# Performance work log

Measured on AMD Instinct MI355X. Metric: run time of the kernel, lower is better.

The kernel has to match this reference:

```python
import jax, jax.numpy as jnp
import numpy as np

SEQ_LENS = [1024, 768, 512, 896, 640, 384, 1024, 896]
TOTAL = sum(SEQ_LENS)  # 6144
EMBED = 768
NUM_HEADS = 12
HEAD_DIM = EMBED // NUM_HEADS
FFN = 3072
LN_EPS = 1e-5


def _pad_maps():
    # static (numpy) index maps for ragged <-> padded layout
    B, S = len(SEQ_LENS), max(SEQ_LENS)
    offs = np.cumsum([0] + SEQ_LENS)
    pad_idx = np.zeros((B, S), np.int32)
    valid = np.zeros((B, S), bool)
    for i, L in enumerate(SEQ_LENS):
        pad_idx[i, :L] = np.arange(offs[i], offs[i] + L)
        valid[i, :L] = True
    flat_b = np.concatenate([np.full(L, i, np.int32) for i, L in enumerate(SEQ_LENS)])
    flat_p = np.concatenate([np.arange(L, dtype=np.int32) for L in SEQ_LENS])
    return jnp.asarray(pad_idx), jnp.asarray(valid), jnp.asarray(flat_b), jnp.asarray(flat_p)

PAD_IDX, VALID, FLAT_B, FLAT_P = _pad_maps()


def _layernorm(x, g, b):
    mu = jnp.mean(x, axis=-1, keepdims=True)
    var = jnp.mean(jnp.square(x - mu), axis=-1, keepdims=True)
    return (x - mu) * jax.lax.rsqrt(var + LN_EPS) * g + b


def setup_inputs() -> dict:
    key = jax.random.key(0)
    ks = jax.random.split(key, 8)
    return {
        "hidden_states": jax.random.normal(ks[0], (TOTAL, EMBED), jnp.float32),
        "attention_mask": jnp.ones((TOTAL,), jnp.int32),
        "in_proj_w": 0.02 * jax.random.normal(ks[1], (3 * EMBED, EMBED), jnp.float32),
        "in_proj_b": jnp.zeros((3 * EMBED,), jnp.float32),
        "out_proj_w": 0.02 * jax.random.normal(ks[2], (EMBED, EMBED), jnp.float32),
        "out_proj_b": jnp.zeros((EMBED,), jnp.float32),
        "ln1_g": jnp.ones((EMBED,), jnp.float32),
        "ln1_b": jnp.zeros((EMBED,), jnp.float32),
        "fc1_w": 0.02 * jax.random.normal(ks[3], (FFN, EMBED), jnp.float32),
        "fc1_b": jnp.zeros((FFN,), jnp.float32),
        "fc2_w": 0.02 * jax.random.normal(ks[4], (EMBED, FFN), jnp.float32),
        "fc2_b": jnp.zeros((EMBED,), jnp.float32),
        "ln2_g": jnp.ones((EMBED,), jnp.float32),
        "ln2_b": jnp.zeros((EMBED,), jnp.float32),
    }


def reference(hidden_states, attention_mask, in_proj_w, in_proj_b, out_proj_w,
              out_proj_b, ln1_g, ln1_b, fc1_w, fc1_b, fc2_w, fc2_b, ln2_g, ln2_b):
    B, S = PAD_IDX.shape
    residual = hidden_states
    x = _layernorm(hidden_states, ln1_g, ln1_b)  # pre-LN (do_layer_norm_before)

    # ragged -> padded [B, S, E]; key validity combines padding mask and ragged tail
    xp = x[PAD_IDX]
    key_valid = VALID & (attention_mask[PAD_IDX] != 0)

    # fused QKV projection (nn.MultiheadAttention in_proj)
    qkv = xp @ in_proj_w.T + in_proj_b  # [B, S, 3E]
    q, k, v = jnp.split(qkv, 3, axis=-1)
    q = q.reshape(B, S, NUM_HEADS, HEAD_DIM) * (1.0 / np.sqrt(HEAD_DIM))
    k = k.reshape(B, S, NUM_HEADS, HEAD_DIM)
    v = v.reshape(B, S, NUM_HEADS, HEAD_DIM)

    scores = jnp.einsum('bqhd,bkhd->bhqk', q, k)  # [B, H, S, S]
    causal = jnp.tril(jnp.ones((S, S), bool))
    mask = causal[None, None] & key_valid[:, None, None, :]
    scores = jnp.where(mask, scores, jnp.float32(-1e30))
    probs = jax.nn.softmax(scores, axis=-1)
    ctx = jnp.einsum('bhqk,bkhd->bqhd', probs, v).reshape(B, S, EMBED)
    attn = ctx @ out_proj_w.T + out_proj_b

    # padded -> ragged, residual
    h = residual + attn[FLAT_B, FLAT_P]

    # FFN block (pre-LN)
    residual = h
    h = _layernorm(h, ln2_g, ln2_b)
    h = jax.nn.relu(h @ fc1_w.T + fc1_b)
    h = h @ fc2_w.T + fc2_b
    return residual + h
```

## Files before the change

kernel.cpp:

```cpp
#include <hip/hip_runtime.h>
#include <hip/hip_bf16.h>

#define TOTAL 6144
#define EMBED 768
#define QKV3  2304
#define FFN   3072
#define NH    12
#define HD    64

typedef unsigned short u16;
typedef unsigned int u32;
typedef float f32x4 __attribute__((ext_vector_type(4)));
typedef __bf16 bf16x8 __attribute__((ext_vector_type(8)));

__device__ __constant__ int BOFF[9] = {0, 1024, 1792, 2304, 3200, 3840, 4224, 5248, 6144};

__device__ __forceinline__ float b2f(u16 h) {
    union { u32 u; float f; } v; v.u = ((u32)h) << 16; return v.f;
}
__device__ __forceinline__ u16 f2b(float f) {
    union { u32 u; float f; } v; v.f = f;
    u32 u = v.u + 0x7fffu + ((v.u >> 16) & 1u);
    return (u16)(u >> 16);
}

__device__ __forceinline__ void gload_lds16(const u16* g, u16* l) {
    __builtin_amdgcn_global_load_lds(
        (const __attribute__((address_space(1))) u32*)(uintptr_t)g,
        (__attribute__((address_space(3))) u32*)(uintptr_t)l, 16, 0, 0);
}

__device__ __forceinline__ float rowmax16(float x) {
    int v;
    v = __builtin_amdgcn_mov_dpp(__float_as_int(x), 0xB1, 0xF, 0xF, true);
    x = fmaxf(x, __int_as_float(v));
    v = __builtin_amdgcn_mov_dpp(__float_as_int(x), 0x4E, 0xF, 0xF, true);
    x = fmaxf(x, __int_as_float(v));
    v = __builtin_amdgcn_mov_dpp(__float_as_int(x), 0x124, 0xF, 0xF, true);
    x = fmaxf(x, __int_as_float(v));
    v = __builtin_amdgcn_mov_dpp(__float_as_int(x), 0x128, 0xF, 0xF, true);
    x = fmaxf(x, __int_as_float(v));
    return x;
}

__global__ void cvt4_kernel(const float* __restrict__ s0, u16* __restrict__ d0, int n0,
                            const float* __restrict__ s1, u16* __restrict__ d1, int n1,
                            const float* __restrict__ s2, u16* __restrict__ d2, int n2,
                            const float* __restrict__ s3, u16* __restrict__ d3, int n3) {
    int i = blockIdx.x * blockDim.x + threadIdx.x;
    const float* s;
    u16* d;
    int j = i;
    if (j < n0) { s = s0; d = d0; }
    else {
        j -= n0;
        if (j < n1) { s = s1; d = d1; }
        else {
            j -= n1;
            if (j < n2) { s = s2; d = d2; }
            else {
                j -= n2;
                if (j >= n3) return;
                s = s3; d = d3;
            }
        }
    }
    float4 v = ((const float4*)s)[j];
    ushort4 o;
    o.x = f2b(v.x); o.y = f2b(v.y); o.z = f2b(v.z); o.w = f2b(v.w);
    ((ushort4*)d)[j] = o;
}

__global__ __launch_bounds__(256) void ln_kernel(const float* __restrict__ x,
                                                 const float* __restrict__ g,
                                                 const float* __restrict__ b,
                                                 u16* __restrict__ out) {
    int row = blockIdx.x * 4 + (threadIdx.x >> 6);
    int lane = threadIdx.x & 63;
    const float* xr = x + (size_t)row * EMBED;
    float4 v[3];
    float s = 0.f, sq = 0.f;
#pragma unroll
    for (int c = 0; c < 3; ++c) {
        v[c] = *(const float4*)(xr + c * 256 + lane * 4);
        s += v[c].x + v[c].y + v[c].z + v[c].w;
        sq += v[c].x * v[c].x + v[c].y * v[c].y + v[c].z * v[c].z + v[c].w * v[c].w;
    }
#pragma unroll
    for (int o = 32; o; o >>= 1) {
        s += __shfl_xor(s, o);
        sq += __shfl_xor(sq, o);
    }
    float mu = s * (1.f / 768.f);
    float var = sq * (1.f / 768.f) - mu * mu;
    float rs = rsqrtf(var + 1e-5f);
    u16* orow = out + (size_t)row * EMBED;
#pragma unroll
    for (int c = 0; c < 3; ++c) {
        int col = c * 256 + lane * 4;
        float4 gg = *(const float4*)(g + col);
        float4 bb = *(const float4*)(b + col);
        ushort4 o;
        o.x = f2b((v[c].x - mu) * rs * gg.x + bb.x);
        o.y = f2b((v[c].y - mu) * rs * gg.y + bb.y);
        o.z = f2b((v[c].z - mu) * rs * gg.z + bb.z);
        o.w = f2b((v[c].w - mu) * rs * gg.w + bb.w);
        *(ushort4*)(orow + col) = o;
    }
}

template <int RELU, int RES, int OUTB, int OUTF>
__global__ __launch_bounds__(256) void gemm128(const u16* __restrict__ A,
                                               const u16* __restrict__ B,
                                               const float* __restrict__ bias,
                                               const float* __restrict__ res,
                                               u16* __restrict__ outb,
                                               float* __restrict__ outf,
                                               int M, int N, int K) {
    __shared__ u16 As[2][128][64];
    __shared__ u16 Bs[2][128][64];
    int t = threadIdx.x;
    int lane = t & 63, w = t >> 6;
    int wr = w >> 1, wc = w & 1;
    int gx = gridDim.x;
    int nwg = gx * gridDim.y;
    int flat = blockIdx.y * gx + blockIdx.x;
    int swz = (flat & 7) * (nwg >> 3) + (flat >> 3);
    int m0 = (swz / gx) * 128, n0 = (swz % gx) * 128;
    int lr = lane >> 3;
    int lcg = (lane & 7) ^ (lr & 7);
    int c16 = lane & 15, hi = lane >> 4;

    f32x4 acc[4][4];
#pragma unroll
    for (int m = 0; m < 4; ++m)
#pragma unroll
        for (int n = 0; n < 4; ++n) acc[m][n] = (f32x4)0.f;

    const u16* Ab = A + (size_t)(m0 + w * 32 + lr) * K + lcg * 8;
    const u16* Bb = B + (size_t)(n0 + w * 32 + lr) * K + lcg * 8;

    int nk = K >> 6;
#pragma unroll
    for (int i = 0; i < 4; ++i) {
        gload_lds16(Ab + (size_t)(i * 8) * K, &As[0][w * 32 + i * 8][0]);
        gload_lds16(Bb + (size_t)(i * 8) * K, &Bs[0][w * 32 + i * 8][0]);
    }

    for (int tk = 0; tk < nk; ++tk) {
        int cur = tk & 1;
        if (tk + 1 < nk) {
            int k1 = (tk + 1) << 6;
#pragma unroll
            for (int i = 0; i < 4; ++i) {
                gload_lds16(Ab + (size_t)(i * 8) * K + k1, &As[cur ^ 1][w * 32 + i * 8][0]);
                gload_lds16(Bb + (size_t)(i * 8) * K + k1, &Bs[cur ^ 1][w * 32 + i * 8][0]);
            }
            asm volatile("s_waitcnt vmcnt(8)" ::: "memory");
        } else {
            asm volatile("s_waitcnt vmcnt(0)" ::: "memory");
        }
        __builtin_amdgcn_sched_barrier(0);
        __builtin_amdgcn_s_barrier();
#pragma unroll
        for (int ks = 0; ks < 2; ++ks) {
            bf16x8 af[4], bfr[4];
#pragma unroll
            for (int m = 0; m < 4; ++m)
                af[m] = *(const bf16x8*)&As[cur][wr * 64 + m * 16 + c16][((ks * 4 + hi) ^ (c16 & 7)) * 8];
#pragma unroll
            for (int n = 0; n < 4; ++n)
                bfr[n] = *(const bf16x8*)&Bs[cur][wc * 64 + n * 16 + c16][((ks * 4 + hi) ^ (c16 & 7)) * 8];
#pragma unroll
            for (int m = 0; m < 4; ++m)
#pragma unroll
                for (int n = 0; n < 4; ++n)
                    acc[m][n] = __builtin_amdgcn_mfma_f32_16x16x32_bf16(af[m], bfr[n], acc[m][n], 0, 0, 0);
        }
        asm volatile("s_waitcnt lgkmcnt(0)" ::: "memory");
        __builtin_amdgcn_sched_barrier(0);
        __builtin_amdgcn_s_barrier();
    }

#pragma unroll
    for (int m = 0; m < 4; ++m)
#pragma unroll
        for (int n = 0; n < 4; ++n) {
            int cg = n0 + wc * 64 + n * 16 + c16;
            float bv = bias[cg];
#pragma unroll
            for (int j = 0; j < 4; ++j) {
                int rg = m0 + wr * 64 + m * 16 + hi * 4 + j;
                float v = acc[m][n][j] + bv;
                if (RELU) v = fmaxf(v, 0.f);
                if (RES) v += res[(size_t)rg * N + cg];
                if (OUTB) outb[(size_t)rg * N + cg] = f2b(v);
                if (OUTF) outf[(size_t)rg * N + cg] = v;
            }
        }
}

__global__ __launch_bounds__(256) void vtrans_kernel(const u16* __restrict__ qkv,
                                                     u16* __restrict__ vT) {
    __shared__ u16 T[64][64];
    int t = threadIdx.x;
    int r0 = blockIdx.x * 64;
    int d0 = blockIdx.y * 64;
#pragma unroll
    for (int s = 0; s < 2; ++s) {
        int idx = s * 256 + t;
        int r = idx >> 3, cg = idx & 7;
        uint4 v = *(const uint4*)&qkv[(size_t)(r0 + r) * QKV3 + 2 * EMBED + d0 + cg * 8];
        int sw = (((r & 7) ^ ((r >> 3) & 7)) << 3);
        *(uint4*)&T[r][(cg * 8) ^ sw] = v;
    }
    __syncthreads();
#pragma unroll
    for (int s = 0; s < 2; ++s) {
        int idx = s * 256 + t;
        int gd = idx >> 3, rc = idx & 7;
        u16 tmp[8];
#pragma unroll
        for (int j = 0; j < 8; ++j) {
            int row = rc * 8 + j;
            int sw = (((row & 7) ^ ((row >> 3) & 7)) << 3);
            tmp[j] = T[row][gd ^ sw];
        }
        *(uint4*)&vT[(size_t)(d0 + gd) * TOTAL + r0 + rc * 8] = *(uint4*)tmp;
    }
}

__global__ __launch_bounds__(64, 2) void attn_mfma(const u16* __restrict__ qkv,
                                                   const u16* __restrict__ vT,
                                                   const int* __restrict__ amask,
                                                   u16* __restrict__ ctx) {
    __shared__ u16 Pl[32][64];
    int l = threadIdx.x;
    int Q = l >> 4, c = l & 15;
    int bid = blockIdx.x;
    int swz = (bid & 7) * 288 + (bid >> 3);
    int h = swz / 192;
    int qt = 191 - (swz % 192);
    int r0 = qt * 32;
    int b = 0;
#pragma unroll
    for (int i = 0; i < 8; ++i)
        if (r0 >= BOFF[i + 1]) b = i + 1;
    int boff = BOFF[b];
    int p0 = r0 - boff;
    int nk = p0 + 32;
    const float SCALE = 0.125f * 1.44269504f;

    bf16x8 qa[2][2];
#pragma unroll
    for (int m = 0; m < 2; ++m)
#pragma unroll
        for (int ks = 0; ks < 2; ++ks)
            qa[m][ks] = *(const bf16x8*)&qkv[(size_t)(r0 + m * 16 + c) * QKV3 + h * HD + ks * 32 + Q * 8];

    bf16x8 vones;
#pragma unroll
    for (int j = 0; j < 8; ++j) vones[j] = (__bf16)1.0f;

    f32x4 oacc[2][4], lacc[2];
    float mrun[2][4];
#pragma unroll
    for (int m = 0; m < 2; ++m) {
        lacc[m] = (f32x4)0.f;
#pragma unroll
        for (int nt = 0; nt < 4; ++nt) oacc[m][nt] = (f32x4)0.f;
#pragma unroll
        for (int r = 0; r < 4; ++r) mrun[m][r] = -1e30f;
    }

    for (int k0 = 0; k0 < nk; k0 += 64) {
        bf16x8 kb[2][4], vb[2][4];
#pragma unroll
        for (int ks = 0; ks < 2; ++ks)
#pragma unroll
            for (int nt = 0; nt < 4; ++nt) {
                kb[ks][nt] = *(const bf16x8*)&qkv[(size_t)(boff + k0 + nt * 16 + c) * QKV3 +
                                                  EMBED + h * HD + ks * 32 + Q * 8];
                vb[ks][nt] = *(const bf16x8*)&vT[(size_t)(h * HD + nt * 16 + c) * TOTAL +
                                                 boff + k0 + ks * 32 + Q * 8];
            }

        f32x4 sacc[2][4];
#pragma unroll
        for (int m = 0; m < 2; ++m)
#pragma unroll
            for (int nt = 0; nt < 4; ++nt) sacc[m][nt] = (f32x4)0.f;
#pragma unroll
        for (int ks = 0; ks < 2; ++ks)
#pragma unroll
            for (int m = 0; m < 2; ++m)
#pragma unroll
                for (int nt = 0; nt < 4; ++nt)
                    sacc[m][nt] = __builtin_amdgcn_mfma_f32_16x16x32_bf16(qa[m][ks], kb[ks][nt], sacc[m][nt], 0, 0, 0);

        int am[4];
#pragma unroll
        for (int nt = 0; nt < 4; ++nt) am[nt] = amask[boff + k0 + nt * 16 + c];
#pragma unroll
        for (int m = 0; m < 2; ++m)
#pragma unroll
            for (int nt = 0; nt < 4; ++nt) {
                int kpos = k0 + nt * 16 + c;
                float madd = am[nt] ? 0.f : -1e30f;
#pragma unroll
                for (int r = 0; r < 4; ++r) {
                    float s = fmaf(sacc[m][nt][r], SCALE, madd);
                    int qp = p0 + m * 16 + 4 * Q + r;
                    sacc[m][nt][r] = (kpos <= qp) ? s : -1e30f;
                }
            }

        float mx[2][4];
        int small = 1;
#pragma unroll
        for (int m = 0; m < 2; ++m)
#pragma unroll
            for (int r = 0; r < 4; ++r) {
                float v = fmaxf(fmaxf(sacc[m][0][r], sacc[m][1][r]),
                                fmaxf(sacc[m][2][r], sacc[m][3][r]));
                v = rowmax16(v);
                mx[m][r] = v;
                small &= (v <= mrun[m][r]) ? 1 : 0;
            }
        if (!__all(small)) {
#pragma unroll
            for (int m = 0; m < 2; ++m)
#pragma unroll
                for (int r = 0; r < 4; ++r) {
                    float mn = fmaxf(mrun[m][r], mx[m][r]);
                    float f = exp2f(mrun[m][r] - mn);
                    mrun[m][r] = mn;
                    lacc[m][r] *= f;
#pragma unroll
                    for (int nt = 0; nt < 4; ++nt) oacc[m][nt][r] *= f;
                }
        }

#pragma unroll
        for (int m = 0; m < 2; ++m)
#pragma unroll
            for (int nt = 0; nt < 4; ++nt)
#pragma unroll
                for (int r = 0; r < 4; ++r) {
                    float p = exp2f(sacc[m][nt][r] - mrun[m][r]);
                    int row = m * 16 + 4 * Q + r;
                    int cch = ((nt * 2 + (c >> 3)) ^ (row & 7)) << 3;
                    Pl[row][cch + (c & 7)] = f2b(p);
                }

#pragma unroll
        for (int ks = 0; ks < 2; ++ks) {
            bf16x8 pa[2];
#pragma unroll
            for (int m = 0; m < 2; ++m)
                pa[m] = *(const bf16x8*)&Pl[m * 16 + c][(((ks * 4 + Q) ^ (c & 7)) << 3)];
#pragma unroll
            for (int m = 0; m < 2; ++m) {
                lacc[m] = __builtin_amdgcn_mfma_f32_16x16x32_bf16(pa[m], vones, lacc[m], 0, 0, 0);
#pragma unroll
                for (int nt = 0; nt < 4; ++nt)
                    oacc[m][nt] = __builtin_amdgcn_mfma_f32_16x16x32_bf16(pa[m], vb[ks][nt], oacc[m][nt], 0, 0, 0);
            }
        }
    }

#pragma unroll
    for (int m = 0; m < 2; ++m)
#pragma unroll
        for (int r = 0; r < 4; ++r) {
            float inv = 1.0f / lacc[m][r];
#pragma unroll
            for (int nt = 0; nt < 4; ++nt)
                ctx[(size_t)(r0 + m * 16 + 4 * Q + r) * EMBED + h * HD + nt * 16 + c] =
                    f2b(oacc[m][nt][r] * inv);
        }
}

extern "C" void kernel_launch(void* const* d_in, const int* in_sizes, int n_in,
                              void* d_out, int out_size, void* d_ws, size_t ws_size,
                              hipStream_t stream) {
    (void)in_sizes; (void)n_in; (void)out_size; (void)ws_size;
    const float* hidden = (const float*)d_in[0];
    const int*   amask  = (const int*)d_in[1];
    const float* in_w   = (const float*)d_in[2];
    const float* in_b   = (const float*)d_in[3];
    const float* out_w  = (const float*)d_in[4];
    const float* out_b  = (const float*)d_in[5];
    const float* ln1g   = (const float*)d_in[6];
    const float* ln1b   = (const float*)d_in[7];
    const float* fc1w   = (const float*)d_in[8];
    const float* fc1b   = (const float*)d_in[9];
    const float* fc2w   = (const float*)d_in[10];
    const float* fc2b   = (const float*)d_in[11];
    const float* ln2g   = (const float*)d_in[12];
    const float* ln2b   = (const float*)d_in[13];
    float* out = (float*)d_out;

    char* ws = (char*)d_ws;
    size_t off = 0;
    auto alloc = [&](size_t bytes) {
        void* p = ws + off;
        off += (bytes + 255) & ~(size_t)255;
        return p;
    };
    u16* w_in_bf  = (u16*)alloc((size_t)QKV3 * EMBED * 2);
    u16* w_out_bf = (u16*)alloc((size_t)EMBED * EMBED * 2);
    u16* w_fc1_bf = (u16*)alloc((size_t)FFN * EMBED * 2);
    u16* w_fc2_bf = (u16*)alloc((size_t)EMBED * FFN * 2);
    u16* xln  = (u16*)alloc((size_t)TOTAL * EMBED * 2);
    u16* qkv  = (u16*)alloc((size_t)TOTAL * QKV3 * 2);
    u16* ctx  = (u16*)alloc((size_t)TOTAL * EMBED * 2);
    float* hmid = (float*)alloc((size_t)TOTAL * EMBED * 4);
    u16* hln  = (u16*)alloc((size_t)TOTAL * EMBED * 2);
    u16* f1o  = (u16*)alloc((size_t)TOTAL * FFN * 2);
    u16* vT   = xln;

    cvt4_kernel<<<6912, 256, 0, stream>>>(in_w, w_in_bf, 442368,
                                          out_w, w_out_bf, 147456,
                                          fc1w, w_fc1_bf, 589824,
                                          fc2w, w_fc2_bf, 589824);

    ln_kernel<<<TOTAL / 4, 256, 0, stream>>>(hidden, ln1g, ln1b, xln);
    gemm128<0, 0, 1, 0><<<dim3(QKV3 / 128, TOTAL / 128), 256, 0, stream>>>(
        xln, w_in_bf, in_b, nullptr, qkv, nullptr, TOTAL, QKV3, EMBED);
    vtrans_kernel<<<dim3(TOTAL / 64, EMBED / 64), 256, 0, stream>>>(qkv, vT);
    attn_mfma<<<dim3((TOTAL / 32) * NH), 64, 0, stream>>>(qkv, vT, amask, ctx);
    gemm128<0, 1, 0, 1><<<dim3(EMBED / 128, TOTAL / 128), 256, 0, stream>>>(
        ctx, w_out_bf, out_b, hidden, nullptr, hmid, TOTAL, EMBED, EMBED);
    ln_kernel<<<TOTAL / 4, 256, 0, stream>>>(hmid, ln2g, ln2b, hln);
    gemm128<1, 0, 1, 0><<<dim3(FFN / 128, TOTAL / 128), 256, 0, stream>>>(
        hln, w_fc1_bf, fc1b, nullptr, f1o, nullptr, TOTAL, FFN, EMBED);
    gemm128<0, 1, 0, 1><<<dim3(EMBED / 128, TOTAL / 128), 256, 0, stream>>>(
        f1o, w_fc2_bf, fc2b, hmid, nullptr, out, TOTAL, EMBED, FFN);
}
```

Measured before the change: 227.3 us.

## Split attention key loop across four waves with LDS softmax combine

Attention blocks grow from one wave to four. Each wave processes an interleaved subset of 64-key chunks with its own online-softmax state. Partial outputs, running maxima and sums are then merged through shared memory before writing the context. The goal is to shorten the serial key loop for long causal rows and expose more parallelism per query tile. In exchange it adds a reduction step, two barriers and about 35KB of LDS per block, and leaves waves idle on short tiles.

```diff
diff --git a/kernel.cpp b/kernel.cpp
--- a/kernel.cpp
+++ b/kernel.cpp
@@ -230,12 +230,21 @@
     }
 }
 
-__global__ __launch_bounds__(64, 2) void attn_mfma(const u16* __restrict__ qkv,
-                                                   const u16* __restrict__ vT,
-                                                   const int* __restrict__ amask,
-                                                   u16* __restrict__ ctx) {
-    __shared__ u16 Pl[32][64];
-    int l = threadIdx.x;
+struct CombineBufs {
+    float om[4][64][33];
+    float ml[4][32][2];
+};
+union AttnLds {
+    u16 pl[4][32][64];
+    CombineBufs c;
+};
+
+__global__ __launch_bounds__(256) void attn_mfma(const u16* __restrict__ qkv,
+                                                 const u16* __restrict__ vT,
+                                                 const int* __restrict__ amask,
+                                                 u16* __restrict__ ctx) {
+    __shared__ AttnLds S;
+    int t = threadIdx.x, l = t & 63, w = t >> 6;
     int Q = l >> 4, c = l & 15;
     int bid = blockIdx.x;
     int swz = (bid & 7) * 288 + (bid >> 3);
@@ -273,7 +282,8 @@
         for (int r = 0; r < 4; ++r) mrun[m][r] = -1e30f;
     }
 
-    for (int k0 = 0; k0 < nk; k0 += 64) {
+    for (int kc = w; (kc << 6) < nk; kc += 4) {
+        int k0 = kc << 6;
         bf16x8 kb[2][4], vb[2][4];
 #pragma unroll
         for (int ks = 0; ks < 2; ++ks)
@@ -350,7 +360,7 @@
                     float p = exp2f(sacc[m][nt][r] - mrun[m][r]);
                     int row = m * 16 + 4 * Q + r;
                     int cch = ((nt * 2 + (c >> 3)) ^ (row & 7)) << 3;
-                    Pl[row][cch + (c & 7)] = f2b(p);
+                    S.pl[w][row][cch + (c & 7)] = f2b(p);
                 }
 
 #pragma unroll
@@ -358,7 +368,7 @@
             bf16x8 pa[2];
 #pragma unroll
             for (int m = 0; m < 2; ++m)
-                pa[m] = *(const bf16x8*)&Pl[m * 16 + c][(((ks * 4 + Q) ^ (c & 7)) << 3)];
+                pa[m] = *(const bf16x8*)&S.pl[w][m * 16 + c][(((ks * 4 + Q) ^ (c & 7)) << 3)];
 #pragma unroll
             for (int m = 0; m < 2; ++m) {
                 lacc[m] = __builtin_amdgcn_mfma_f32_16x16x32_bf16(pa[m], vones, lacc[m], 0, 0, 0);
@@ -369,16 +379,52 @@
         }
     }
 
+    __syncthreads();
 #pragma unroll
     for (int m = 0; m < 2; ++m)
 #pragma unroll
+        for (int nt = 0; nt < 4; ++nt)
+            *(f32x4*)&S.c.om[w][nt * 16 + c][m * 16 + 4 * Q] = oacc[m][nt];
+    if (c == 0) {
+#pragma unroll
+        for (int m = 0; m < 2; ++m)
+#pragma unroll
+            for (int r = 0; r < 4; ++r) {
+                int row = m * 16 + 4 * Q + r;
+                S.c.ml[w][row][0] = mrun[m][r];
+                S.c.ml[w][row][1] = lacc[m][r];
+            }
+    }
+    __syncthreads();
+
+#pragma unroll
+    for (int m = 0; m < 2; ++m) {
+        int rbase = m * 16 + 4 * Q;
+        float Mm[4], ll[4];
+#pragma unroll
         for (int r = 0; r < 4; ++r) {
-            float inv = 1.0f / lacc[m][r];
-#pragma unroll
-            for (int nt = 0; nt < 4; ++nt)
-                ctx[(size_t)(r0 + m * 16 + 4 * Q + r) * EMBED + h * HD + nt * 16 + c] =
-                    f2b(oacc[m][nt][r] * inv);
-        }
+            float mm = -1e30f;
+#pragma unroll
+            for (int wv = 0; wv < 4; ++wv) mm = fmaxf(mm, S.c.ml[wv][rbase + r][0]);
+            Mm[r] = mm;
+            float lt = 0.f;
+#pragma unroll
+            for (int wv = 0; wv < 4; ++wv)
+                lt += exp2f(S.c.ml[wv][rbase + r][0] - mm) * S.c.ml[wv][rbase + r][1];
+            ll[r] = lt;
+        }
+        f32x4 o = (f32x4)0.f;
+#pragma unroll
+        for (int wv = 0; wv < 4; ++wv) {
+            f32x4 ov = *(const f32x4*)&S.c.om[wv][w * 16 + c][rbase];
+#pragma unroll
+            for (int r = 0; r < 4; ++r)
+                o[r] += exp2f(S.c.ml[wv][rbase + r][0] - Mm[r]) * ov[r];
+        }
+#pragma unroll
+        for (int r = 0; r < 4; ++r)
+            ctx[(size_t)(r0 + rbase + r) * EMBED + h * HD + w * 16 + c] = f2b(o[r] / ll[r]);
+    }
 }
 
 extern "C" void kernel_launch(void* const* d_in, const int* in_sizes, int n_in,
@@ -429,7 +475,7 @@
     gemm128<0, 0, 1, 0><<<dim3(QKV3 / 128, TOTAL / 128), 256, 0, stream>>>(
         xln, w_in_bf, in_b, nullptr, qkv, nullptr, TOTAL, QKV3, EMBED);
     vtrans_kernel<<<dim3(TOTAL / 64, EMBED / 64), 256, 0, stream>>>(qkv, vT);
-    attn_mfma<<<dim3((TOTAL / 32) * NH), 64, 0, stream>>>(qkv, vT, amask, ctx);
+    attn_mfma<<<dim3((TOTAL / 32) * NH), 256, 0, stream>>>(qkv, vT, amask, ctx);
     gemm128<0, 1, 0, 1><<<dim3(EMBED / 128, TOTAL / 128), 256, 0, stream>>>(
         ctx, w_out_bf, out_b, hidden, nullptr, hmid, TOTAL, EMBED, EMBED);
     ln_kernel<<<TOTAL / 4, 256, 0, stream>>>(hmid, ln2g, ln2b, hln);
```

Result: no change. 230.3 us (+1.3%).

## Double-buffer K/V loads in attention, bitpack mask, skip causal masking on full chunks

Applied to the files above, without the earlier changes.

Restructures the attention inner loop to prefetch the next K/V chunk into a second register set while the current chunk computes. The int attention mask is packed into bitmasks by a new small kernel, and mask and causal work is skipped on chunks that lie fully below the diagonal when no keys are masked. The scale is folded into the exp2 argument, and the row sum comes from DPP reductions instead of an extra MFMA with a ones vector. The bf16 conversion now uses the native cast. Prefetching doubles the K/V register footprint, which may raise register pressure and hurt occupancy.

```diff
diff --git a/kernel.cpp b/kernel.cpp
--- a/kernel.cpp
+++ b/kernel.cpp
@@ -15,13 +15,9 @@
 
 __device__ __constant__ int BOFF[9] = {0, 1024, 1792, 2304, 3200, 3840, 4224, 5248, 6144};
 
-__device__ __forceinline__ float b2f(u16 h) {
-    union { u32 u; float f; } v; v.u = ((u32)h) << 16; return v.f;
-}
 __device__ __forceinline__ u16 f2b(float f) {
-    union { u32 u; float f; } v; v.f = f;
-    u32 u = v.u + 0x7fffu + ((v.u >> 16) & 1u);
-    return (u16)(u >> 16);
+    __bf16 h = (__bf16)f;
+    return __builtin_bit_cast(u16, h);
 }
 
 __device__ __forceinline__ void gload_lds16(const u16* g, u16* l) {
@@ -40,6 +36,18 @@
     x = fmaxf(x, __int_as_float(v));
     v = __builtin_amdgcn_mov_dpp(__float_as_int(x), 0x128, 0xF, 0xF, true);
     x = fmaxf(x, __int_as_float(v));
+    return x;
+}
+__device__ __forceinline__ float rowsum16(float x) {
+    int v;
+    v = __builtin_amdgcn_mov_dpp(__float_as_int(x), 0xB1, 0xF, 0xF, true);
+    x += __int_as_float(v);
+    v = __builtin_amdgcn_mov_dpp(__float_as_int(x), 0x4E, 0xF, 0xF, true);
+    x += __int_as_float(v);
+    v = __builtin_amdgcn_mov_dpp(__float_as_int(x), 0x124, 0xF, 0xF, true);
+    x += __int_as_float(v);
+    v = __builtin_amdgcn_mov_dpp(__float_as_int(x), 0x128, 0xF, 0xF, true);
+    x += __int_as_float(v);
     return x;
 }
 
@@ -69,6 +77,15 @@
     ushort4 o;
     o.x = f2b(v.x); o.y = f2b(v.y); o.z = f2b(v.z); o.w = f2b(v.w);
     ((ushort4*)d)[j] = o;
+}
+
+__global__ void maskbits_kernel(const int* __restrict__ am, u32* __restrict__ mb) {
+    int i = blockIdx.x * 64 + threadIdx.x;
+    unsigned long long bal = __ballot(am[i] != 0);
+    if (threadIdx.x == 0) {
+        mb[blockIdx.x * 2] = (u32)bal;
+        mb[blockIdx.x * 2 + 1] = (u32)(bal >> 32);
+    }
 }
 
 __global__ __launch_bounds__(256) void ln_kernel(const float* __restrict__ x,
@@ -232,11 +249,11 @@
 
 __global__ __launch_bounds__(64, 2) void attn_mfma(const u16* __restrict__ qkv,
                                                    const u16* __restrict__ vT,
-                                                   const int* __restrict__ amask,
+                                                   const u32* __restrict__ mbits,
                                                    u16* __restrict__ ctx) {
     __shared__ u16 Pl[32][64];
     int l = threadIdx.x;
-    int Q = l >> 4, c = l & 15;
+    int hi = l >> 4, c = l & 15;
     int bid = blockIdx.x;
     int swz = (bid & 7) * 288 + (bid >> 3);
     int h = swz / 192;
@@ -248,7 +265,8 @@
         if (r0 >= BOFF[i + 1]) b = i + 1;
     int boff = BOFF[b];
     int p0 = r0 - boff;
-    int nk = p0 + 32;
+    int nchunks = (p0 >> 6) + 1;
+    int nfull = (p0 >= 63) ? (((p0 - 63) >> 6) + 1) : 0;
     const float SCALE = 0.125f * 1.44269504f;
 
     bf16x8 qa[2][2];
@@ -256,35 +274,40 @@
     for (int m = 0; m < 2; ++m)
 #pragma unroll
         for (int ks = 0; ks < 2; ++ks)
-            qa[m][ks] = *(const bf16x8*)&qkv[(size_t)(r0 + m * 16 + c) * QKV3 + h * HD + ks * 32 + Q * 8];
-
-    bf16x8 vones;
-#pragma unroll
-    for (int j = 0; j < 8; ++j) vones[j] = (__bf16)1.0f;
-
-    f32x4 oacc[2][4], lacc[2];
-    float mrun[2][4];
-#pragma unroll
-    for (int m = 0; m < 2; ++m) {
-        lacc[m] = (f32x4)0.f;
+            qa[m][ks] = *(const bf16x8*)&qkv[(size_t)(r0 + m * 16 + c) * QKV3 + h * HD + ks * 32 + hi * 8];
+
+    f32x4 oacc[2][4];
+    float lacc[2][4], mrun[2][4];
+#pragma unroll
+    for (int m = 0; m < 2; ++m)
+#pragma unroll
+        for (int r = 0; r < 4; ++r) {
+            lacc[m][r] = 0.f;
+            mrun[m][r] = -1e30f;
+        }
+#pragma unroll
+    for (int m = 0; m < 2; ++m)
 #pragma unroll
         for (int nt = 0; nt < 4; ++nt) oacc[m][nt] = (f32x4)0.f;
-#pragma unroll
-        for (int r = 0; r < 4; ++r) mrun[m][r] = -1e30f;
-    }
-
-    for (int k0 = 0; k0 < nk; k0 += 64) {
-        bf16x8 kb[2][4], vb[2][4];
+
+    auto loadc = [&](int kc, bf16x8 (&kb)[2][4], bf16x8 (&vb)[2][4], u32 (&mw)[2]) {
+        int k0 = kc << 6;
 #pragma unroll
         for (int ks = 0; ks < 2; ++ks)
 #pragma unroll
             for (int nt = 0; nt < 4; ++nt) {
                 kb[ks][nt] = *(const bf16x8*)&qkv[(size_t)(boff + k0 + nt * 16 + c) * QKV3 +
-                                                  EMBED + h * HD + ks * 32 + Q * 8];
+                                                  EMBED + h * HD + ks * 32 + hi * 8];
                 vb[ks][nt] = *(const bf16x8*)&vT[(size_t)(h * HD + nt * 16 + c) * TOTAL +
-                                                 boff + k0 + ks * 32 + Q * 8];
+                                                 boff + k0 + ks * 32 + hi * 8];
             }
-
+        int wi = (boff + k0) >> 5;
+        mw[0] = mbits[wi];
+        mw[1] = mbits[wi + 1];
+    };
+
+    auto body = [&](int kc, bf16x8 (&kb)[2][4], bf16x8 (&vb)[2][4], u32 (&mw)[2]) {
+        int k0 = kc << 6;
         f32x4 sacc[2][4];
 #pragma unroll
         for (int m = 0; m < 2; ++m)
@@ -298,22 +321,31 @@
                 for (int nt = 0; nt < 4; ++nt)
                     sacc[m][nt] = __builtin_amdgcn_mfma_f32_16x16x32_bf16(qa[m][ks], kb[ks][nt], sacc[m][nt], 0, 0, 0);
 
-        int am[4];
-#pragma unroll
-        for (int nt = 0; nt < 4; ++nt) am[nt] = amask[boff + k0 + nt * 16 + c];
-#pragma unroll
-        for (int m = 0; m < 2; ++m)
-#pragma unroll
-            for (int nt = 0; nt < 4; ++nt) {
-                int kpos = k0 + nt * 16 + c;
-                float madd = am[nt] ? 0.f : -1e30f;
-#pragma unroll
-                for (int r = 0; r < 4; ++r) {
-                    float s = fmaf(sacc[m][nt][r], SCALE, madd);
-                    int qp = p0 + m * 16 + 4 * Q + r;
-                    sacc[m][nt][r] = (kpos <= qp) ? s : -1e30f;
+        bool fullmask = ((mw[0] & mw[1]) == 0xFFFFFFFFu);
+        if (kc >= nfull) {
+#pragma unroll
+            for (int m = 0; m < 2; ++m)
+#pragma unroll
+                for (int nt = 0; nt < 4; ++nt) {
+                    int kpos = k0 + nt * 16 + c;
+                    float madd = fullmask ? 0.f
+                        : (((mw[nt >> 1] >> (((nt & 1) << 4) + c)) & 1u) ? 0.f : -1e30f);
+#pragma unroll
+                    for (int r = 0; r < 4; ++r) {
+                        int qp = p0 + m * 16 + 4 * hi + r;
+                        sacc[m][nt][r] = (kpos <= qp) ? (sacc[m][nt][r] + madd) : -1e30f;
+                    }
                 }
-            }
+        } else if (!fullmask) {
+#pragma unroll
+            for (int m = 0; m < 2; ++m)
+#pragma unroll
+                for (int nt = 0; nt < 4; ++nt) {
+                    float madd = ((mw[nt >> 1] >> (((nt & 1) << 4) + c)) & 1u) ? 0.f : -1e30f;
+#pragma unroll
+                    for (int r = 0; r < 4; ++r) sacc[m][nt][r] += madd;
+                }
+        }
 
         float mx[2][4];
         int small = 1;
@@ -333,7 +365,7 @@
 #pragma unroll
                 for (int r = 0; r < 4; ++r) {
                     float mn = fmaxf(mrun[m][r], mx[m][r]);
-                    float f = exp2f(mrun[m][r] - mn);
+                    float f = exp2f((mrun[m][r] - mn) * SCALE);
                     mrun[m][r] = mn;
                     lacc[m][r] *= f;
 #pragma unroll
@@ -341,32 +373,58 @@
                 }
         }
 
+        float negm[2][4];
 #pragma unroll
         for (int m = 0; m < 2; ++m)
 #pragma unroll
+            for (int r = 0; r < 4; ++r) negm[m][r] = -mrun[m][r] * SCALE;
+        float psum[2][4];
+#pragma unroll
+        for (int m = 0; m < 2; ++m)
+#pragma unroll
+            for (int r = 0; r < 4; ++r) psum[m][r] = 0.f;
+#pragma unroll
+        for (int m = 0; m < 2; ++m)
+#pragma unroll
             for (int nt = 0; nt < 4; ++nt)
 #pragma unroll
                 for (int r = 0; r < 4; ++r) {
-                    float p = exp2f(sacc[m][nt][r] - mrun[m][r]);
-                    int row = m * 16 + 4 * Q + r;
+                    float p = exp2f(fmaf(sacc[m][nt][r], SCALE, negm[m][r]));
+                    psum[m][r] += p;
+                    int row = m * 16 + 4 * hi + r;
                     int cch = ((nt * 2 + (c >> 3)) ^ (row & 7)) << 3;
                     Pl[row][cch + (c & 7)] = f2b(p);
                 }
+#pragma unroll
+        for (int m = 0; m < 2; ++m)
+#pragma unroll
+            for (int r = 0; r < 4; ++r) lacc[m][r] += rowsum16(psum[m][r]);
 
 #pragma unroll
         for (int ks = 0; ks < 2; ++ks) {
             bf16x8 pa[2];
 #pragma unroll
             for (int m = 0; m < 2; ++m)
-                pa[m] = *(const bf16x8*)&Pl[m * 16 + c][(((ks * 4 + Q) ^ (c & 7)) << 3)];
-#pragma unroll
-            for (int m = 0; m < 2; ++m) {
-                lacc[m] = __builtin_amdgcn_mfma_f32_16x16x32_bf16(pa[m], vones, lacc[m], 0, 0, 0);
+                pa[m] = *(const bf16x8*)&Pl[m * 16 + c][(((ks * 4 + hi) ^ (c & 7)) << 3)];
+#pragma unroll
+            for (int m = 0; m < 2; ++m)
 #pragma unroll
                 for (int nt = 0; nt < 4; ++nt)
                     oacc[m][nt] = __builtin_amdgcn_mfma_f32_16x16x32_bf16(pa[m], vb[ks][nt], oacc[m][nt], 0, 0, 0);
-            }
-        }
+        }
+    };
+
+    bf16x8 kbA[2][4], vbA[2][4], kbB[2][4], vbB[2][4];
+    u32 mwA[2], mwB[2];
+    loadc(0, kbA, vbA, mwA);
+    int kc = 0;
+    while (true) {
+        if (kc + 1 < nchunks) loadc(kc + 1, kbB, vbB, mwB);
+        body(kc, kbA, vbA, mwA);
+        if (++kc >= nchunks) break;
+        if (kc + 1 < nchunks) loadc(kc + 1, kbA, vbA, mwA);
+        body(kc, kbB, vbB, mwB);
+        if (++kc >= nchunks) break;
     }
 
 #pragma unroll
@@ -376,7 +434,7 @@
             float inv = 1.0f / lacc[m][r];
 #pragma unroll
             for (int nt = 0; nt < 4; ++nt)
-                ctx[(size_t)(r0 + m * 16 + 4 * Q + r) * EMBED + h * HD + nt * 16 + c] =
+                ctx[(size_t)(r0 + m * 16 + 4 * hi + r) * EMBED + h * HD + nt * 16 + c] =
                     f2b(oacc[m][nt][r] * inv);
         }
 }
@@ -418,18 +476,20 @@
     float* hmid = (float*)alloc((size_t)TOTAL * EMBED * 4);
     u16* hln  = (u16*)alloc((size_t)TOTAL * EMBED * 2);
     u16* f1o  = (u16*)alloc((size_t)TOTAL * FFN * 2);
+    u32* mbits = (u32*)alloc(192 * 4);
     u16* vT   = xln;
 
     cvt4_kernel<<<6912, 256, 0, stream>>>(in_w, w_in_bf, 442368,
                                           out_w, w_out_bf, 147456,
                                           fc1w, w_fc1_bf, 589824,
                                           fc2w, w_fc2_bf, 589824);
+    maskbits_kernel<<<96, 64, 0, stream>>>(amask, mbits);
 
     ln_kernel<<<TOTAL / 4, 256, 0, stream>>>(hidden, ln1g, ln1b, xln);
     gemm128<0, 0, 1, 0><<<dim3(QKV3 / 128, TOTAL / 128), 256, 0, stream>>>(
         xln, w_in_bf, in_b, nullptr, qkv, nullptr, TOTAL, QKV3, EMBED);
     vtrans_kernel<<<dim3(TOTAL / 64, EMBED / 64), 256, 0, stream>>>(qkv, vT);
-    attn_mfma<<<dim3((TOTAL / 32) * NH), 64, 0, stream>>>(qkv, vT, amask, ctx);
+    attn_mfma<<<dim3((TOTAL / 32) * NH), 64, 0, stream>>>(qkv, vT, mbits, ctx);
     gemm128<0, 1, 0, 1><<<dim3(EMBED / 128, TOTAL / 128), 256, 0, stream>>>(
         ctx, w_out_bf, out_b, hidden, nullptr, hmid, TOTAL, EMBED, EMBED);
     ln_kernel<<<TOTAL / 4, 256, 0, stream>>>(hmid, ln2g, ln2b, hln);
```

New measurement: 266.7 us. +17.3%, slower.

## Fuse V transpose into QKV GEMM epilogue and bitpack attention mask

Applied to the files above, without the earlier changes.

Removes the separate V-transpose kernel by having the QKV GEMM epilogue write V transposed directly into a spare buffer. Precomputes the attention mask as bitwords with a ballot kernel, and skips causal and mask arithmetic for fully-below-diagonal chunks when the mask word is all ones. It also folds the softmax scale into the exp2 FMA and uses the hardware bf16 conversion. The cost is scattered 8-byte strided stores in the GEMM epilogue and an extra tiny launch.

```diff
diff --git a/kernel.cpp b/kernel.cpp
--- a/kernel.cpp
+++ b/kernel.cpp
@@ -15,13 +15,9 @@
 
 __device__ __constant__ int BOFF[9] = {0, 1024, 1792, 2304, 3200, 3840, 4224, 5248, 6144};
 
-__device__ __forceinline__ float b2f(u16 h) {
-    union { u32 u; float f; } v; v.u = ((u32)h) << 16; return v.f;
-}
 __device__ __forceinline__ u16 f2b(float f) {
-    union { u32 u; float f; } v; v.f = f;
-    u32 u = v.u + 0x7fffu + ((v.u >> 16) & 1u);
-    return (u16)(u >> 16);
+    __bf16 h = (__bf16)f;
+    return __builtin_bit_cast(u16, h);
 }
 
 __device__ __forceinline__ void gload_lds16(const u16* g, u16* l) {
@@ -71,6 +67,15 @@
     ((ushort4*)d)[j] = o;
 }
 
+__global__ void maskbits_kernel(const int* __restrict__ am, u32* __restrict__ mb) {
+    int i = blockIdx.x * 64 + threadIdx.x;
+    unsigned long long bal = __ballot(am[i] != 0);
+    if (threadIdx.x == 0) {
+        mb[blockIdx.x * 2] = (u32)bal;
+        mb[blockIdx.x * 2 + 1] = (u32)(bal >> 32);
+    }
+}
+
 __global__ __launch_bounds__(256) void ln_kernel(const float* __restrict__ x,
                                                  const float* __restrict__ g,
                                                  const float* __restrict__ b,
@@ -109,13 +114,14 @@
     }
 }
 
-template <int RELU, int RES, int OUTB, int OUTF>
+template <int RELU, int RES, int OUTB, int OUTF, int VTR>
 __global__ __launch_bounds__(256) void gemm128(const u16* __restrict__ A,
                                                const u16* __restrict__ B,
                                                const float* __restrict__ bias,
                                                const float* __restrict__ res,
                                                u16* __restrict__ outb,
                                                float* __restrict__ outf,
+                                               u16* __restrict__ vout,
                                                int M, int N, int K) {
     __shared__ u16 As[2][128][64];
     __shared__ u16 Bs[2][128][64];
@@ -188,55 +194,33 @@
         for (int n = 0; n < 4; ++n) {
             int cg = n0 + wc * 64 + n * 16 + c16;
             float bv = bias[cg];
+            float vj[4];
 #pragma unroll
             for (int j = 0; j < 4; ++j) {
                 int rg = m0 + wr * 64 + m * 16 + hi * 4 + j;
                 float v = acc[m][n][j] + bv;
                 if (RELU) v = fmaxf(v, 0.f);
                 if (RES) v += res[(size_t)rg * N + cg];
+                vj[j] = v;
                 if (OUTB) outb[(size_t)rg * N + cg] = f2b(v);
                 if (OUTF) outf[(size_t)rg * N + cg] = v;
             }
-        }
-}
-
-__global__ __launch_bounds__(256) void vtrans_kernel(const u16* __restrict__ qkv,
-                                                     u16* __restrict__ vT) {
-    __shared__ u16 T[64][64];
-    int t = threadIdx.x;
-    int r0 = blockIdx.x * 64;
-    int d0 = blockIdx.y * 64;
-#pragma unroll
-    for (int s = 0; s < 2; ++s) {
-        int idx = s * 256 + t;
-        int r = idx >> 3, cg = idx & 7;
-        uint4 v = *(const uint4*)&qkv[(size_t)(r0 + r) * QKV3 + 2 * EMBED + d0 + cg * 8];
-        int sw = (((r & 7) ^ ((r >> 3) & 7)) << 3);
-        *(uint4*)&T[r][(cg * 8) ^ sw] = v;
-    }
-    __syncthreads();
-#pragma unroll
-    for (int s = 0; s < 2; ++s) {
-        int idx = s * 256 + t;
-        int gd = idx >> 3, rc = idx & 7;
-        u16 tmp[8];
-#pragma unroll
-        for (int j = 0; j < 8; ++j) {
-            int row = rc * 8 + j;
-            int sw = (((row & 7) ^ ((row >> 3) & 7)) << 3);
-            tmp[j] = T[row][gd ^ sw];
-        }
-        *(uint4*)&vT[(size_t)(d0 + gd) * TOTAL + r0 + rc * 8] = *(uint4*)tmp;
-    }
+            if (VTR && cg >= 2 * EMBED) {
+                ushort4 tv;
+                tv.x = f2b(vj[0]); tv.y = f2b(vj[1]); tv.z = f2b(vj[2]); tv.w = f2b(vj[3]);
+                int rgb = m0 + wr * 64 + m * 16 + hi * 4;
+                *(ushort4*)&vout[(size_t)(cg - 2 * EMBED) * TOTAL + rgb] = tv;
+            }
+        }
 }
 
 __global__ __launch_bounds__(64, 2) void attn_mfma(const u16* __restrict__ qkv,
                                                    const u16* __restrict__ vT,
-                                                   const int* __restrict__ amask,
+                                                   const u32* __restrict__ mbits,
                                                    u16* __restrict__ ctx) {
     __shared__ u16 Pl[32][64];
     int l = threadIdx.x;
-    int Q = l >> 4, c = l & 15;
+    int hi = l >> 4, c = l & 15;
     int bid = blockIdx.x;
     int swz = (bid & 7) * 288 + (bid >> 3);
     int h = swz / 192;
@@ -248,7 +232,8 @@
         if (r0 >= BOFF[i + 1]) b = i + 1;
     int boff = BOFF[b];
     int p0 = r0 - boff;
-    int nk = p0 + 32;
+    int nchunks = (p0 >> 6) + 1;
+    int nfull = (p0 >= 63) ? (((p0 - 63) >> 6) + 1) : 0;
     const float SCALE = 0.125f * 1.44269504f;
 
     bf16x8 qa[2][2];
@@ -256,7 +241,7 @@
     for (int m = 0; m < 2; ++m)
 #pragma unroll
         for (int ks = 0; ks < 2; ++ks)
-            qa[m][ks] = *(const bf16x8*)&qkv[(size_t)(r0 + m * 16 + c) * QKV3 + h * HD + ks * 32 + Q * 8];
+            qa[m][ks] = *(const bf16x8*)&qkv[(size_t)(r0 + m * 16 + c) * QKV3 + h * HD + ks * 32 + hi * 8];
 
     bf16x8 vones;
 #pragma unroll
@@ -273,17 +258,20 @@
         for (int r = 0; r < 4; ++r) mrun[m][r] = -1e30f;
     }
 
-    for (int k0 = 0; k0 < nk; k0 += 64) {
+    for (int kc = 0; kc < nchunks; ++kc) {
+        int k0 = kc << 6;
         bf16x8 kb[2][4], vb[2][4];
 #pragma unroll
         for (int ks = 0; ks < 2; ++ks)
 #pragma unroll
             for (int nt = 0; nt < 4; ++nt) {
                 kb[ks][nt] = *(const bf16x8*)&qkv[(size_t)(boff + k0 + nt * 16 + c) * QKV3 +
-                                                  EMBED + h * HD + ks * 32 + Q * 8];
+                                                  EMBED + h * HD + ks * 32 + hi * 8];
                 vb[ks][nt] = *(const bf16x8*)&vT[(size_t)(h * HD + nt * 16 + c) * TOTAL +
-                                                 boff + k0 + ks * 32 + Q * 8];
-            }
+                                                 boff + k0 + ks * 32 + hi * 8];
+            }
+        int wi = (boff + k0) >> 5;
+        u32 mw0 = mbits[wi], mw1 = mbits[wi + 1];
 
         f32x4 sacc[2][4];
 #pragma unroll
@@ -298,22 +286,33 @@
                 for (int nt = 0; nt < 4; ++nt)
                     sacc[m][nt] = __builtin_amdgcn_mfma_f32_16x16x32_bf16(qa[m][ks], kb[ks][nt], sacc[m][nt], 0, 0, 0);
 
-        int am[4];
-#pragma unroll
-        for (int nt = 0; nt < 4; ++nt) am[nt] = amask[boff + k0 + nt * 16 + c];
-#pragma unroll
-        for (int m = 0; m < 2; ++m)
-#pragma unroll
-            for (int nt = 0; nt < 4; ++nt) {
-                int kpos = k0 + nt * 16 + c;
-                float madd = am[nt] ? 0.f : -1e30f;
-#pragma unroll
-                for (int r = 0; r < 4; ++r) {
-                    float s = fmaf(sacc[m][nt][r], SCALE, madd);
-                    int qp = p0 + m * 16 + 4 * Q + r;
-                    sacc[m][nt][r] = (kpos <= qp) ? s : -1e30f;
+        bool fullmask = ((mw0 & mw1) == 0xFFFFFFFFu);
+        if (kc >= nfull) {
+#pragma unroll
+            for (int m = 0; m < 2; ++m)
+#pragma unroll
+                for (int nt = 0; nt < 4; ++nt) {
+                    int kpos = k0 + nt * 16 + c;
+                    u32 mwv = (nt & 2) ? mw1 : mw0;
+                    float madd = fullmask ? 0.f
+                        : (((mwv >> (((nt & 1) << 4) + c)) & 1u) ? 0.f : -1e30f);
+#pragma unroll
+                    for (int r = 0; r < 4; ++r) {
+                        int qp = p0 + m * 16 + 4 * hi + r;
+                        sacc[m][nt][r] = (kpos <= qp) ? (sacc[m][nt][r] + madd) : -1e30f;
+                    }
                 }
-            }
+        } else if (!fullmask) {
+#pragma unroll
+            for (int m = 0; m < 2; ++m)
+#pragma unroll
+                for (int nt = 0; nt < 4; ++nt) {
+                    u32 mwv = (nt & 2) ? mw1 : mw0;
+                    float madd = ((mwv >> (((nt & 1) << 4) + c)) & 1u) ? 0.f : -1e30f;
+#pragma unroll
+                    for (int r = 0; r < 4; ++r) sacc[m][nt][r] += madd;
+                }
+        }
 
         float mx[2][4];
         int small = 1;
@@ -333,7 +332,7 @@
 #pragma unroll
                 for (int r = 0; r < 4; ++r) {
                     float mn = fmaxf(mrun[m][r], mx[m][r]);
-                    float f = exp2f(mrun[m][r] - mn);
+                    float f = exp2f((mrun[m][r] - mn) * SCALE);
                     mrun[m][r] = mn;
                     lacc[m][r] *= f;
 #pragma unroll
@@ -341,14 +340,19 @@
                 }
         }
 
+        float negm[2][4];
 #pragma unroll
         for (int m = 0; m < 2; ++m)
 #pragma unroll
+            for (int r = 0; r < 4; ++r) negm[m][r] = -mrun[m][r] * SCALE;
+#pragma unroll
+        for (int m = 0; m < 2; ++m)
+#pragma unroll
             for (int nt = 0; nt < 4; ++nt)
 #pragma unroll
                 for (int r = 0; r < 4; ++r) {
-                    float p = exp2f(sacc[m][nt][r] - mrun[m][r]);
-                    int row = m * 16 + 4 * Q + r;
+                    float p = exp2f(fmaf(sacc[m][nt][r], SCALE, negm[m][r]));
+                    int row = m * 16 + 4 * hi + r;
                     int cch = ((nt * 2 + (c >> 3)) ^ (row & 7)) << 3;
                     Pl[row][cch + (c & 7)] = f2b(p);
                 }
@@ -358,7 +362,7 @@
             bf16x8 pa[2];
 #pragma unroll
             for (int m = 0; m < 2; ++m)
-                pa[m] = *(const bf16x8*)&Pl[m * 16 + c][(((ks * 4 + Q) ^ (c & 7)) << 3)];
+                pa[m] = *(const bf16x8*)&Pl[m * 16 + c][(((ks * 4 + hi) ^ (c & 7)) << 3)];
 #pragma unroll
             for (int m = 0; m < 2; ++m) {
                 lacc[m] = __builtin_amdgcn_mfma_f32_16x16x32_bf16(pa[m], vones, lacc[m], 0, 0, 0);
@@ -376,7 +380,7 @@
             float inv = 1.0f / lacc[m][r];
 #pragma unroll
             for (int nt = 0; nt < 4; ++nt)
-                ctx[(size_t)(r0 + m * 16 + 4 * Q + r) * EMBED + h * HD + nt * 16 + c] =
+                ctx[(size_t)(r0 + m * 16 + 4 * hi + r) * EMBED + h * HD + nt * 16 + c] =
                     f2b(oacc[m][nt][r] * inv);
         }
 }
@@ -418,23 +422,24 @@
     float* hmid = (float*)alloc((size_t)TOTAL * EMBED * 4);
     u16* hln  = (u16*)alloc((size_t)TOTAL * EMBED * 2);
     u16* f1o  = (u16*)alloc((size_t)TOTAL * FFN * 2);
-    u16* vT   = xln;
+    u32* mbits = (u32*)alloc(192 * 4);
+    u16* vT = hln;
 
     cvt4_kernel<<<6912, 256, 0, stream>>>(in_w, w_in_bf, 442368,
                                           out_w, w_out_bf, 147456,
                                           fc1w, w_fc1_bf, 589824,
                                           fc2w, w_fc2_bf, 589824);
+    maskbits_kernel<<<96, 64, 0, stream>>>(amask, mbits);
 
     ln_kernel<<<TOTAL / 4, 256, 0, stream>>>(hidden, ln1g, ln1b, xln);
-    gemm128<0, 0, 1, 0><<<dim3(QKV3 / 128, TOTAL / 128), 256, 0, stream>>>(
-        xln, w_in_bf, in_b, nullptr, qkv, nullptr, TOTAL, QKV3, EMBED);
-    vtrans_kernel<<<dim3(TOTAL / 64, EMBED / 64), 256, 0, stream>>>(qkv, vT);
-    attn_mfma<<<dim3((TOTAL / 32) * NH), 64, 0, stream>>>(qkv, vT, amask, ctx);
-    gemm128<0, 1, 0, 1><<<dim3(EMBED / 128, TOTAL / 128), 256, 0, stream>>>(
-        ctx, w_out_bf, out_b, hidden, nullptr, hmid, TOTAL, EMBED, EMBED);
+    gemm128<0, 0, 1, 0, 1><<<dim3(QKV3 / 128, TOTAL / 128), 256, 0, stream>>>(
+        xln, w_in_bf, in_b, nullptr, qkv, nullptr, vT, TOTAL, QKV3, EMBED);
+    attn_mfma<<<dim3((TOTAL / 32) * NH), 64, 0, stream>>>(qkv, vT, mbits, ctx);
+    gemm128<0, 1, 0, 1, 0><<<dim3(EMBED / 128, TOTAL / 128), 256, 0, stream>>>(
+        ctx, w_out_bf, out_b, hidden, nullptr, hmid, nullptr, TOTAL, EMBED, EMBED);
     ln_kernel<<<TOTAL / 4, 256, 0, stream>>>(hmid, ln2g, ln2b, hln);
-    gemm128<1, 0, 1, 0><<<dim3(FFN / 128, TOTAL / 128), 256, 0, stream>>>(
-        hln, w_fc1_bf, fc1b, nullptr, f1o, nullptr, TOTAL, FFN, EMBED);
-    gemm128<0, 1, 0, 1><<<dim3(EMBED / 128, TOTAL / 128), 256, 0, stream>>>(
-        f1o, w_fc2_bf, fc2b, hmid, nullptr, out, TOTAL, EMBED, FFN);
-}
+    gemm128<1, 0, 1, 0, 0><<<dim3(FFN / 128, TOTAL / 128), 256, 0, stream>>>(
+        hln, w_fc1_bf, fc1b, nullptr, f1o, nullptr, nullptr, TOTAL, FFN, EMBED);
+    gemm128<0, 1, 0, 1, 0><<<dim3(EMBED / 128, TOTAL / 128), 256, 0, stream>>>(
+        f1o, w_fc2_bf, fc2b, hmid, nullptr, out, nullptr, TOTAL, EMBED, FFN);
+}
```

Measured after the change: 221.8 us. 1.02x faster.
